# Kernel tuning notes

Measured on AMD Instinct MI355X. Metric: run time of the kernel, lower is better.

## Reference

```python
import jax, jax.numpy as jnp
import numpy as np

B, S, D = 8, 2048, 128

def setup_inputs() -> dict:
    key = jax.random.key(0)
    kq, kk, kv, km = jax.random.split(key, 4)
    q = jax.random.normal(kq, (B, S, D), dtype=jnp.float32)
    k = jax.random.normal(kk, (B, S, D), dtype=jnp.float32)
    v = jax.random.normal(kv, (B, S, D), dtype=jnp.float32)
    # True = masked position (torch masked_fill semantics)
    mask = jax.random.bernoulli(km, 0.1, (B, S))
    return {"q": q, "k": k, "v": v, "mask": mask}

def reference(q, k, v, mask):
    # score[b,i,j] = q[b,i,:] . k[b,j,:]  (no 1/sqrt(d) scaling, as in source)
    score = jnp.einsum('bik,bjk->bij', q, k)
    # stable exp: max taken over ALL keys (including masked), matching source order
    score = jnp.exp(score - jnp.max(score, axis=-1, keepdims=True))
    # mask (B,S) broadcasts over query dim; masked keys zeroed AFTER exp
    score = jnp.where(mask[:, None, :], 0.0, score)
    a = score / jnp.sum(score, axis=-1, keepdims=True)
    return jnp.einsum('bij,bjd->bid', a, v)
```

## Files before the change

### kernel.cpp

```cpp
#include <hip/hip_runtime.h>
#include <hip/hip_bf16.h>
#include <stdint.h>

#define B_ 8
#define S_ 2048
#define D_ 128
#define QBLK 64
#define KVB 32
#define SHALF 1024
#define NIT (SHALF / KVB)
#define VST 40

typedef _Float16 f16;
typedef f16 f16x8 __attribute__((ext_vector_type(8)));
typedef f16 f16x4 __attribute__((ext_vector_type(4)));
typedef f16 f16x2 __attribute__((ext_vector_type(2)));
typedef float f32x4 __attribute__((ext_vector_type(4)));

__global__ __launch_bounds__(512, 2) void attn_fwd(const float* __restrict__ Q,
                                                   const float* __restrict__ K,
                                                   const float* __restrict__ V,
                                                   const void* __restrict__ Mp,
                                                   float* __restrict__ O) {
  const int t = threadIdx.x;
  const int b = blockIdx.y;
  const int q0 = blockIdx.x * QBLK;
  const int w = t >> 6, l = t & 63, l15 = l & 15, lg = l >> 4;
  const int rowgrp = w & 3, kvh = w >> 2;

  __shared__ alignas(16) char smem[47360];
  f16* Klds  = (f16*)smem;
  f16* Vt    = (f16*)(smem + 16384);
  f16* Pl    = (f16*)(smem + 36864);
  float* madd = (float*)(smem + 47104);
  float* mrg = (float*)smem;
  float* mlb = (float*)(smem + 36864);

  const uint32_t* mw = (const uint32_t*)Mp;
  int oki = 1, okf = 1;
#pragma unroll
  for (int i = 0; i < 4; ++i) {
    uint32_t x = mw[t * 4 + i];
    oki &= (x <= 1u) ? 1 : 0;
    okf &= (x == 0u || x == 0x3f800000u) ? 1 : 0;
  }
  const int alli = __syncthreads_and(oki);
  const int allf = __syncthreads_and(okf);
  const int mode = alli ? 0 : (allf ? 2 : 1);
  const int*     mi32 = (const int*)Mp + b * S_;
  const uint8_t* mu8  = (const uint8_t*)Mp + b * S_;
  const float*   mf32 = (const float*)Mp + b * S_;

  f16x8 qf[4];
  {
    const int qrow = q0 + 16 * rowgrp + l15;
    const float* qp = Q + ((size_t)b * S_ + qrow) * D_ + lg * 8;
#pragma unroll
    for (int kt = 0; kt < 4; ++kt) {
      float4 a = *(const float4*)(qp + 32 * kt);
      float4 c = *(const float4*)(qp + 32 * kt + 4);
      qf[kt] = (f16x8){(f16)a.x, (f16)a.y, (f16)a.z, (f16)a.w,
                       (f16)c.x, (f16)c.y, (f16)c.z, (f16)c.w};
    }
  }

  f32x4 acco[8];
#pragma unroll
  for (int dt = 0; dt < 8; ++dt) acco[dt] = (f32x4){0.f, 0.f, 0.f, 0.f};
  float m_r = -1e30f, l_r = 0.f;

  const float* Kb = K + (size_t)b * S_ * D_;
  const float* Vb = V + (size_t)b * S_ * D_;
  const int kc4 = (t & 31) * 4;
  const int kgr = t >> 5;
  const int vc  = (t >> 4) * 4;
  const int vkp = t & 15;

  float4 kreg[4], vreg[4];
  float mreg = 0.f;

#define LOADT(KV0)                                                                    \
  {                                                                                   \
    _Pragma("unroll") for (int p = 0; p < 4; ++p) {                                   \
      const int gr = kgr + 16 * p, half = gr >> 5, row = gr & 31;                     \
      kreg[p] = *(const float4*)(Kb + (size_t)(half * SHALF + (KV0) + row) * D_ + kc4); \
    }                                                                                 \
    _Pragma("unroll") for (int p = 0; p < 2; ++p) {                                   \
      const int kg = vkp + 16 * p, half = kg >> 4, kp = kg & 15;                      \
      const float* vp = Vb + (size_t)(half * SHALF + (KV0) + 2 * kp) * D_ + vc;       \
      vreg[2 * p]     = *(const float4*)vp;                                           \
      vreg[2 * p + 1] = *(const float4*)(vp + D_);                                    \
    }                                                                                 \
    if (t < 64) {                                                                     \
      const int gk = (t >> 5) * SHALF + (KV0) + (t & 31);                             \
      mreg = (mode == 0) ? (mi32[gk] ? 1.f : 0.f)                                     \
           : (mode == 1) ? (mu8[gk] ? 1.f : 0.f) : mf32[gk];                          \
    }                                                                                 \
  }

  LOADT(0);

  for (int it = 0; it < NIT; ++it) {
    const int kv0 = it * KVB;
#pragma unroll
    for (int p = 0; p < 4; ++p) {
      const int gr = kgr + 16 * p, half = gr >> 5, row = gr & 31;
      const int idx = half * 4096 + ((row * 128 + kc4) ^ ((row & 7) << 3));
      float4 kv = kreg[p];
      *(f16x4*)(Klds + idx) = (f16x4){(f16)kv.x, (f16)kv.y, (f16)kv.z, (f16)kv.w};
    }
#pragma unroll
    for (int p = 0; p < 2; ++p) {
      const int kg = vkp + 16 * p, half = kg >> 4, kp = kg & 15;
      float4 v0 = vreg[2 * p], v1 = vreg[2 * p + 1];
#pragma unroll
      for (int i = 0; i < 4; ++i)
        *(f16x2*)(Vt + half * 5120 + (vc + i) * VST + 2 * kp) =
            (f16x2){(f16)(&v0.x)[i], (f16)(&v1.x)[i]};
    }
    if (t < 64) madd[t] = (mreg != 0.f) ? -1e30f : 0.f;
    __syncthreads();

    if (it + 1 < NIT) LOADT(kv0 + KVB);

    f32x4 sacc0 = (f32x4){0.f, 0.f, 0.f, 0.f};
    f32x4 sacc1 = (f32x4){0.f, 0.f, 0.f, 0.f};
#pragma unroll
    for (int kt = 0; kt < 4; ++kt) {
      const int col = lg * 8 + 32 * kt, swz = (l15 & 7) << 3;
      f16x8 kf0 = *(const f16x8*)(Klds + kvh * 4096 + ((l15 * 128 + col) ^ swz));
      f16x8 kf1 = *(const f16x8*)(Klds + kvh * 4096 + (((l15 + 16) * 128 + col) ^ swz));
      sacc0 = __builtin_amdgcn_mfma_f32_16x16x32_f16(kf0, qf[kt], sacc0, 0, 0, 0);
      sacc1 = __builtin_amdgcn_mfma_f32_16x16x32_f16(kf1, qf[kt], sacc1, 0, 0, 0);
    }

    f32x4 ma0 = *(const f32x4*)(madd + kvh * 32 + 4 * lg);
    f32x4 ma1 = *(const f32x4*)(madd + kvh * 32 + 16 + 4 * lg);
    f32x4 s0 = sacc0 + ma0, s1 = sacc1 + ma1;
    float tm = fmaxf(fmaxf(fmaxf(s0[0], s0[1]), fmaxf(s0[2], s0[3])),
                     fmaxf(fmaxf(s1[0], s1[1]), fmaxf(s1[2], s1[3])));
    tm = fmaxf(tm, __shfl_xor(tm, 16));
    tm = fmaxf(tm, __shfl_xor(tm, 32));
    const float mn = fmaxf(m_r, tm);
    const float scale = __expf(m_r - mn);
    m_r = mn;
    float p0[4], p1[4];
#pragma unroll
    for (int r = 0; r < 4; ++r) { p0[r] = __expf(s0[r] - mn); p1[r] = __expf(s1[r] - mn); }
    float rs = (p0[0] + p0[1]) + (p0[2] + p0[3]) + (p1[0] + p1[1]) + (p1[2] + p1[3]);
    rs += __shfl_xor(rs, 16);
    rs += __shfl_xor(rs, 32);
    l_r = l_r * scale + rs;
    *(f16x4*)(Pl + w * 640 + l15 * VST + 4 * lg) =
        (f16x4){(f16)p0[0], (f16)p0[1], (f16)p0[2], (f16)p0[3]};
    *(f16x4*)(Pl + w * 640 + l15 * VST + 16 + 4 * lg) =
        (f16x4){(f16)p1[0], (f16)p1[1], (f16)p1[2], (f16)p1[3]};
    f32x4 scv;
#pragma unroll
    for (int r = 0; r < 4; ++r) scv[r] = __shfl(scale, 4 * lg + r);
#pragma unroll
    for (int dt = 0; dt < 8; ++dt) acco[dt] *= scv;

    f16x8 pa = *(const f16x8*)(Pl + w * 640 + l15 * VST + lg * 8);
#pragma unroll
    for (int dt = 0; dt < 8; ++dt) {
      f16x8 vf = *(const f16x8*)(Vt + kvh * 5120 + (l15 + 16 * dt) * VST + lg * 8);
      acco[dt] = __builtin_amdgcn_mfma_f32_16x16x32_f16(pa, vf, acco[dt], 0, 0, 0);
    }
    __syncthreads();
  }

  if (kvh == 1) {
#pragma unroll
    for (int r = 0; r < 4; ++r) {
      const int row = 4 * lg + r;
#pragma unroll
      for (int dt = 0; dt < 8; ++dt)
        mrg[rowgrp * 2112 + row * 132 + l15 + 16 * dt] = acco[dt][r];
    }
    if (lg == 0) {
      mlb[rowgrp * 32 + l15 * 2]     = m_r;
      mlb[rowgrp * 32 + l15 * 2 + 1] = l_r;
    }
  }
  __syncthreads();
  if (kvh == 0) {
    float m1[4], l1[4];
#pragma unroll
    for (int r = 0; r < 4; ++r) {
      m1[r] = __shfl(m_r, 4 * lg + r);
      l1[r] = __shfl(l_r, 4 * lg + r);
    }
#pragma unroll
    for (int r = 0; r < 4; ++r) {
      const int row = 4 * lg + r;
      const float m2 = mlb[rowgrp * 32 + row * 2];
      const float l2 = mlb[rowgrp * 32 + row * 2 + 1];
      const float mm = fmaxf(m1[r], m2);
      const float e1 = __expf(m1[r] - mm);
      const float e2 = __expf(m2 - mm);
      const float inv = 1.0f / (l1[r] * e1 + l2 * e2);
      float* op = O + ((size_t)b * S_ + q0 + 16 * rowgrp + row) * D_ + l15;
#pragma unroll
      for (int dt = 0; dt < 8; ++dt)
        op[16 * dt] = (acco[dt][r] * e1 + mrg[rowgrp * 2112 + row * 132 + l15 + 16 * dt] * e2) * inv;
    }
  }
}

extern "C" void kernel_launch(void* const* d_in, const int* in_sizes, int n_in,
                              void* d_out, int out_size, void* d_ws, size_t ws_size,
                              hipStream_t stream) {
  const float* q = (const float*)d_in[0];
  const float* k = (const float*)d_in[1];
  const float* v = (const float*)d_in[2];
  const void*  m = d_in[3];
  float* o = (float*)d_out;
  dim3 grid(S_ / QBLK, B_);
  dim3 block(512);
  attn_fwd<<<grid, block, 0, stream>>>(q, k, v, m, o);
}
```

Baseline: 132.6 us.

## Enlarge KV tile to 128 with contiguous halves and reorder grid batch-major

Each iteration now processes 128 keys instead of 32. The two KV-half warp groups take contiguous 64-key slices of the same tile rather than separate sequence halves, which cuts the loop count and with it the number of block barriers. The K load layout, swizzle, V transpose stride and P buffers are rebuilt for the bigger tile, and the grid is flattened so consecutive blocks cover different batches. The cost is roughly double the shared memory (about 88 KB) and more registers for staging, which may lower occupancy below the two blocks per CU the launch bounds request.

```diff
diff --git a/kernel.cpp b/kernel.cpp
--- a/kernel.cpp
+++ b/kernel.cpp
@@ -6,10 +6,9 @@
 #define S_ 2048
 #define D_ 128
 #define QBLK 64
-#define KVB 32
-#define SHALF 1024
-#define NIT (SHALF / KVB)
-#define VST 40
+#define KVB 128
+#define NIT (S_ / KVB)
+#define VST 72
 
 typedef _Float16 f16;
 typedef f16 f16x8 __attribute__((ext_vector_type(8)));
@@ -23,18 +22,19 @@
                                                    const void* __restrict__ Mp,
                                                    float* __restrict__ O) {
   const int t = threadIdx.x;
-  const int b = blockIdx.y;
-  const int q0 = blockIdx.x * QBLK;
+  const int bid = blockIdx.x;
+  const int b = bid & 7;
+  const int q0 = (bid >> 3) * QBLK;
   const int w = t >> 6, l = t & 63, l15 = l & 15, lg = l >> 4;
   const int rowgrp = w & 3, kvh = w >> 2;
 
-  __shared__ alignas(16) char smem[47360];
-  f16* Klds  = (f16*)smem;
-  f16* Vt    = (f16*)(smem + 16384);
-  f16* Pl    = (f16*)(smem + 36864);
-  float* madd = (float*)(smem + 47104);
-  float* mrg = (float*)smem;
-  float* mlb = (float*)(smem + 36864);
+  __shared__ alignas(16) char smem[88576];
+  f16* Klds   = (f16*)smem;
+  f16* Vt     = (f16*)(smem + 32768);
+  f16* Pl     = (f16*)(smem + 69632);
+  float* madd = (float*)(smem + 88064);
+  float* mrg  = (float*)smem;
+  float* mlb  = (float*)(smem + 69632);
 
   const uint32_t* mw = (const uint32_t*)Mp;
   int oki = 1, okf = 1;
@@ -71,101 +71,116 @@
 
   const float* Kb = K + (size_t)b * S_ * D_;
   const float* Vb = V + (size_t)b * S_ * D_;
-  const int kc4 = (t & 31) * 4;
-  const int kgr = t >> 5;
+  const int krow = t >> 2;
+  const int kcol0 = (t & 3) * 32;
   const int vc  = (t >> 4) * 4;
   const int vkp = t & 15;
 
-  float4 kreg[4], vreg[4];
+  float4 kreg[8], vreg[8];
   float mreg = 0.f;
 
-#define LOADT(KV0)                                                                    \
-  {                                                                                   \
-    _Pragma("unroll") for (int p = 0; p < 4; ++p) {                                   \
-      const int gr = kgr + 16 * p, half = gr >> 5, row = gr & 31;                     \
-      kreg[p] = *(const float4*)(Kb + (size_t)(half * SHALF + (KV0) + row) * D_ + kc4); \
-    }                                                                                 \
-    _Pragma("unroll") for (int p = 0; p < 2; ++p) {                                   \
-      const int kg = vkp + 16 * p, half = kg >> 4, kp = kg & 15;                      \
-      const float* vp = Vb + (size_t)(half * SHALF + (KV0) + 2 * kp) * D_ + vc;       \
-      vreg[2 * p]     = *(const float4*)vp;                                           \
-      vreg[2 * p + 1] = *(const float4*)(vp + D_);                                    \
-    }                                                                                 \
-    if (t < 64) {                                                                     \
-      const int gk = (t >> 5) * SHALF + (KV0) + (t & 31);                             \
-      mreg = (mode == 0) ? (mi32[gk] ? 1.f : 0.f)                                     \
-           : (mode == 1) ? (mu8[gk] ? 1.f : 0.f) : mf32[gk];                          \
-    }                                                                                 \
+#define LOADT(KV0)                                                                     \
+  {                                                                                    \
+    _Pragma("unroll") for (int p = 0; p < 8; ++p)                                      \
+      kreg[p] = *(const float4*)(Kb + (size_t)((KV0) + krow) * D_ + kcol0 + 4 * p);    \
+    _Pragma("unroll") for (int p = 0; p < 4; ++p) {                                    \
+      const int g = 2 * (vkp + 16 * p);                                                \
+      const float* vp = Vb + (size_t)((KV0) + g) * D_ + vc;                            \
+      vreg[2 * p]     = *(const float4*)vp;                                            \
+      vreg[2 * p + 1] = *(const float4*)(vp + D_);                                     \
+    }                                                                                  \
+    if (t < KVB) {                                                                     \
+      const int gk = (KV0) + t;                                                        \
+      mreg = (mode == 0) ? (mi32[gk] ? 1.f : 0.f)                                      \
+           : (mode == 1) ? (mu8[gk] ? 1.f : 0.f) : mf32[gk];                           \
+    }                                                                                  \
   }
 
   LOADT(0);
 
   for (int it = 0; it < NIT; ++it) {
-    const int kv0 = it * KVB;
+    {
+      const int half = krow >> 6, r = krow & 63;
+      const int swz = (r & 15) << 3;
+#pragma unroll
+      for (int p = 0; p < 8; ++p) {
+        const int idx = half * 8192 + ((r * 128 + kcol0 + 4 * p) ^ swz);
+        float4 kv = kreg[p];
+        *(f16x4*)(Klds + idx) = (f16x4){(f16)kv.x, (f16)kv.y, (f16)kv.z, (f16)kv.w};
+      }
+    }
 #pragma unroll
     for (int p = 0; p < 4; ++p) {
-      const int gr = kgr + 16 * p, half = gr >> 5, row = gr & 31;
-      const int idx = half * 4096 + ((row * 128 + kc4) ^ ((row & 7) << 3));
-      float4 kv = kreg[p];
-      *(f16x4*)(Klds + idx) = (f16x4){(f16)kv.x, (f16)kv.y, (f16)kv.z, (f16)kv.w};
-    }
-#pragma unroll
-    for (int p = 0; p < 2; ++p) {
-      const int kg = vkp + 16 * p, half = kg >> 4, kp = kg & 15;
+      const int g = 2 * (vkp + 16 * p), half = g >> 6, gl = g & 63;
       float4 v0 = vreg[2 * p], v1 = vreg[2 * p + 1];
 #pragma unroll
       for (int i = 0; i < 4; ++i)
-        *(f16x2*)(Vt + half * 5120 + (vc + i) * VST + 2 * kp) =
+        *(f16x2*)(Vt + half * 9216 + (vc + i) * VST + gl) =
             (f16x2){(f16)(&v0.x)[i], (f16)(&v1.x)[i]};
     }
-    if (t < 64) madd[t] = (mreg != 0.f) ? -1e30f : 0.f;
+    if (t < KVB) madd[t] = (mreg != 0.f) ? -1e30f : 0.f;
     __syncthreads();
 
-    if (it + 1 < NIT) LOADT(kv0 + KVB);
-
-    f32x4 sacc0 = (f32x4){0.f, 0.f, 0.f, 0.f};
-    f32x4 sacc1 = (f32x4){0.f, 0.f, 0.f, 0.f};
-#pragma unroll
-    for (int kt = 0; kt < 4; ++kt) {
-      const int col = lg * 8 + 32 * kt, swz = (l15 & 7) << 3;
-      f16x8 kf0 = *(const f16x8*)(Klds + kvh * 4096 + ((l15 * 128 + col) ^ swz));
-      f16x8 kf1 = *(const f16x8*)(Klds + kvh * 4096 + (((l15 + 16) * 128 + col) ^ swz));
-      sacc0 = __builtin_amdgcn_mfma_f32_16x16x32_f16(kf0, qf[kt], sacc0, 0, 0, 0);
-      sacc1 = __builtin_amdgcn_mfma_f32_16x16x32_f16(kf1, qf[kt], sacc1, 0, 0, 0);
-    }
-
-    f32x4 ma0 = *(const f32x4*)(madd + kvh * 32 + 4 * lg);
-    f32x4 ma1 = *(const f32x4*)(madd + kvh * 32 + 16 + 4 * lg);
-    f32x4 s0 = sacc0 + ma0, s1 = sacc1 + ma1;
-    float tm = fmaxf(fmaxf(fmaxf(s0[0], s0[1]), fmaxf(s0[2], s0[3])),
-                     fmaxf(fmaxf(s1[0], s1[1]), fmaxf(s1[2], s1[3])));
+    if (it + 1 < NIT) LOADT((it + 1) * KVB);
+
+    f32x4 sacc[4];
+#pragma unroll
+    for (int nt = 0; nt < 4; ++nt) sacc[nt] = (f32x4){0.f, 0.f, 0.f, 0.f};
+    const int swzr = l15 << 3;
+#pragma unroll
+    for (int nt = 0; nt < 4; ++nt) {
+#pragma unroll
+      for (int kt = 0; kt < 4; ++kt) {
+        const int idx = kvh * 8192 + (((16 * nt + l15) * 128 + 8 * lg + 32 * kt) ^ swzr);
+        f16x8 kf = *(const f16x8*)(Klds + idx);
+        sacc[nt] = __builtin_amdgcn_mfma_f32_16x16x32_f16(kf, qf[kt], sacc[nt], 0, 0, 0);
+      }
+    }
+
+    f32x4 sm[4];
+#pragma unroll
+    for (int nt = 0; nt < 4; ++nt)
+      sm[nt] = sacc[nt] + *(const f32x4*)(madd + kvh * 64 + 16 * nt + 4 * lg);
+    float q4[4];
+#pragma unroll
+    for (int nt = 0; nt < 4; ++nt)
+      q4[nt] = fmaxf(fmaxf(sm[nt][0], sm[nt][1]), fmaxf(sm[nt][2], sm[nt][3]));
+    float tm = fmaxf(fmaxf(q4[0], q4[1]), fmaxf(q4[2], q4[3]));
     tm = fmaxf(tm, __shfl_xor(tm, 16));
     tm = fmaxf(tm, __shfl_xor(tm, 32));
     const float mn = fmaxf(m_r, tm);
     const float scale = __expf(m_r - mn);
     m_r = mn;
-    float p0[4], p1[4];
-#pragma unroll
-    for (int r = 0; r < 4; ++r) { p0[r] = __expf(s0[r] - mn); p1[r] = __expf(s1[r] - mn); }
-    float rs = (p0[0] + p0[1]) + (p0[2] + p0[3]) + (p1[0] + p1[1]) + (p1[2] + p1[3]);
+    float pv[4][4];
+#pragma unroll
+    for (int nt = 0; nt < 4; ++nt)
+#pragma unroll
+      for (int r = 0; r < 4; ++r) pv[nt][r] = __expf(sm[nt][r] - mn);
+    float rs = ((pv[0][0] + pv[0][1]) + (pv[0][2] + pv[0][3])) +
+               ((pv[1][0] + pv[1][1]) + (pv[1][2] + pv[1][3])) +
+               ((pv[2][0] + pv[2][1]) + (pv[2][2] + pv[2][3])) +
+               ((pv[3][0] + pv[3][1]) + (pv[3][2] + pv[3][3]));
     rs += __shfl_xor(rs, 16);
     rs += __shfl_xor(rs, 32);
     l_r = l_r * scale + rs;
-    *(f16x4*)(Pl + w * 640 + l15 * VST + 4 * lg) =
-        (f16x4){(f16)p0[0], (f16)p0[1], (f16)p0[2], (f16)p0[3]};
-    *(f16x4*)(Pl + w * 640 + l15 * VST + 16 + 4 * lg) =
-        (f16x4){(f16)p1[0], (f16)p1[1], (f16)p1[2], (f16)p1[3]};
+#pragma unroll
+    for (int nt = 0; nt < 4; ++nt)
+      *(f16x4*)(Pl + w * 1152 + l15 * VST + 16 * nt + 4 * lg) =
+          (f16x4){(f16)pv[nt][0], (f16)pv[nt][1], (f16)pv[nt][2], (f16)pv[nt][3]};
     f32x4 scv;
 #pragma unroll
     for (int r = 0; r < 4; ++r) scv[r] = __shfl(scale, 4 * lg + r);
 #pragma unroll
     for (int dt = 0; dt < 8; ++dt) acco[dt] *= scv;
 
-    f16x8 pa = *(const f16x8*)(Pl + w * 640 + l15 * VST + lg * 8);
+    f16x8 pa0 = *(const f16x8*)(Pl + w * 1152 + l15 * VST + 8 * lg);
+    f16x8 pa1 = *(const f16x8*)(Pl + w * 1152 + l15 * VST + 32 + 8 * lg);
 #pragma unroll
     for (int dt = 0; dt < 8; ++dt) {
-      f16x8 vf = *(const f16x8*)(Vt + kvh * 5120 + (l15 + 16 * dt) * VST + lg * 8);
-      acco[dt] = __builtin_amdgcn_mfma_f32_16x16x32_f16(pa, vf, acco[dt], 0, 0, 0);
+      f16x8 vf0 = *(const f16x8*)(Vt + kvh * 9216 + (l15 + 16 * dt) * VST + 8 * lg);
+      f16x8 vf1 = *(const f16x8*)(Vt + kvh * 9216 + (l15 + 16 * dt) * VST + 32 + 8 * lg);
+      acco[dt] = __builtin_amdgcn_mfma_f32_16x16x32_f16(pa0, vf0, acco[dt], 0, 0, 0);
+      acco[dt] = __builtin_amdgcn_mfma_f32_16x16x32_f16(pa1, vf1, acco[dt], 0, 0, 0);
     }
     __syncthreads();
   }
@@ -216,7 +231,7 @@
   const float* v = (const float*)d_in[2];
   const void*  m = d_in[3];
   float* o = (float*)d_out;
-  dim3 grid(S_ / QBLK, B_);
+  dim3 grid((S_ / QBLK) * B_);
   dim3 block(512);
   attn_fwd<<<grid, block, 0, stream>>>(q, k, v, m, o);
 }
```

Result: slower. 151.4 us (+14.2%).
